# Kernel tuning notes

Hardware: AMD Instinct MI355X
Metric: run time of the kernel (lower is better)

## Reference

```python
import jax, jax.numpy as jnp
import numpy as np

N_NODES = 50000


def mean_aggregate(x, src, dst):
    # gather source features, scatter-sum to destinations, divide by in-degree
    msgs = x[src]                                             # [E, D]
    summed = jax.ops.segment_sum(msgs, dst, num_segments=N_NODES)  # [N, D]
    deg = jax.ops.segment_sum(jnp.ones_like(dst, dtype=x.dtype), dst,
                              num_segments=N_NODES)           # [N]
    return summed / jnp.clip(deg, 1.0)[:, None]


def sage_conv(x, src, dst, Wl, Wr, b):
    # PyG SAGEConv (aggr='mean'): lin_l(agg) + lin_r(x); bias only on lin_l
    agg = mean_aggregate(x, src, dst)
    return agg @ Wl + b + x @ Wr


def setup_inputs() -> dict:
    key = jax.random.key(0)
    ks = jax.random.split(key, 8)
    x = jax.random.normal(ks[0], (N_NODES, 64), dtype=jnp.float32)
    edge_index = jax.random.randint(ks[1], (2, 800000), 0, N_NODES, dtype=jnp.int32)
    W1l = jax.random.normal(ks[2], (64, 128), dtype=jnp.float32) * (1.0 / np.sqrt(64))
    W1r = jax.random.normal(ks[3], (64, 128), dtype=jnp.float32) * (1.0 / np.sqrt(64))
    b1 = jnp.zeros((128,), dtype=jnp.float32)
    W2l = jax.random.normal(ks[4], (128, 40), dtype=jnp.float32) * (1.0 / np.sqrt(128))
    W2r = jax.random.normal(ks[5], (128, 40), dtype=jnp.float32) * (1.0 / np.sqrt(128))
    b2 = jnp.zeros((40,), dtype=jnp.float32)
    return {"x": x, "edge_index": edge_index, "W1l": W1l, "W1r": W1r, "b1": b1,
            "W2l": W2l, "W2r": W2r, "b2": b2}


def reference(x, edge_index, W1l, W1r, b1, W2l, W2r, b2):
    src, dst = edge_index[0], edge_index[1]
    h = sage_conv(x, src, dst, W1l, W1r, b1)
    h = jax.nn.relu(h)
    # dropout p=0.5 is identity in eval mode (self.training=False)
    h = sage_conv(h, src, dst, W2l, W2r, b2)
    return h, jax.nn.log_softmax(h, axis=1)
```

## Files before the change

### kernel.cpp

```cpp
#include <hip/hip_runtime.h>
#include <hip/hip_bf16.h>
#include <math.h>

#define N_NODES 50000
#define N_EDGES 800000
#define D0 64
#define D1 128
#define D2 40

#define NB  256
#define NPB 196

typedef short s16x8 __attribute__((ext_vector_type(8)));
typedef float f32x4 __attribute__((ext_vector_type(4)));

static __device__ __forceinline__ unsigned short f2bf(float v) {
    __hip_bfloat16 hb = __float2bfloat16(v);
    return *(unsigned short*)&hb;
}

__global__ __launch_bounds__(256) void prep_kernel(
        const float* __restrict__ x, const int* __restrict__ dst,
        const float* __restrict__ W1l, const float* __restrict__ W1r,
        const float* __restrict__ W2l, const float* __restrict__ W2r,
        unsigned short* __restrict__ xh, int* __restrict__ hist,
        unsigned short* __restrict__ wpk1, unsigned short* __restrict__ wpk2,
        int E, int nCount, int nCast) {
    int b = blockIdx.x, t = threadIdx.x;
    if (b < nCount) {
        __shared__ int h[NB];
        h[t] = 0;
        __syncthreads();
        int e0 = b * 2048;
        for (int i = t; i < 2048; i += 256) {
            int e = e0 + i;
            if (e < E) atomicAdd(&h[(unsigned)dst[e] / NPB], 1);
        }
        __syncthreads();
        hist[b * NB + t] = h[t];
    } else if (b < nCount + nCast) {
        int i = ((b - nCount) * 256 + t) * 4;
        float4 v = *(const float4*)(x + i);
        unsigned o0 = (unsigned)f2bf(v.x) | ((unsigned)f2bf(v.y) << 16);
        unsigned o1 = (unsigned)f2bf(v.z) | ((unsigned)f2bf(v.w) << 16);
        uint2 pk; pk.x = o0; pk.y = o1;
        *(uint2*)(xh + i) = pk;
    } else if (b < nCount + nCast + 8) {
        int f = (b - nCount - nCast) * 4 + (t >> 6);
        int lane = t & 63;
        int nt = f & 7;
        int col = nt * 16 + (lane & 15);
        int kbase = (f >> 3) * 32 + (lane >> 4) * 8;
        unsigned short* o = wpk1 + ((size_t)f * 64 + lane) * 8;
#pragma unroll
        for (int j = 0; j < 8; ++j) {
            int k = kbase + j;
            float w = (k < 64) ? W1r[k * 128 + col] : W1l[(k - 64) * 128 + col];
            o[j] = f2bf(w);
        }
    } else {
        int f = (b - nCount - nCast - 8) * 4 + (t >> 6);
        if (f < 20) {
            int lane = t & 63;
            int nt = f % 5;
            int col = nt * 16 + (lane & 15);
            int kbase = (f / 5) * 32 + (lane >> 4) * 8;
            unsigned short* o = wpk2 + ((size_t)f * 64 + lane) * 8;
#pragma unroll
            for (int j = 0; j < 8; ++j) {
                int k = kbase + j;
                float w = (col < 40) ? W2l[k * 40 + col] : W2r[k * 40 + (col - 40)];
                o[j] = f2bf(w);
            }
        }
    }
}

__global__ void bucket_scan_kernel(const int* __restrict__ hist, int nCount,
                                   int* __restrict__ bbase, int* __restrict__ bcursor) {
    __shared__ int sd[NB];
    int t = threadIdx.x;
    int v = 0;
#pragma unroll 4
    for (int b = 0; b < nCount; ++b) v += hist[b * NB + t];
    sd[t] = v;
    __syncthreads();
    for (int off = 1; off < NB; off <<= 1) {
        int u = (t >= off) ? sd[t - off] : 0;
        __syncthreads();
        sd[t] += u;
        __syncthreads();
    }
    int ex = sd[t] - v;
    bbase[t] = ex;
    bcursor[t] = ex;
}

__global__ __launch_bounds__(256) void bucket_scatter_kernel(
        const int* __restrict__ src, const int* __restrict__ dst,
        int* __restrict__ bcursor, unsigned* __restrict__ ebuf, int E) {
    __shared__ int h[NB];
    __shared__ int base[NB];
    int t = threadIdx.x;
    int e0 = blockIdx.x * 4096;
    h[t] = 0;
    __syncthreads();
    for (int i = t; i < 4096; i += 256) {
        int e = e0 + i;
        if (e < E) atomicAdd(&h[(unsigned)dst[e] / NPB], 1);
    }
    __syncthreads();
    if (h[t] > 0) base[t] = atomicAdd(&bcursor[t], h[t]);
    h[t] = 0;
    __syncthreads();
    for (int i = t; i < 4096; i += 256) {
        int e = e0 + i;
        if (e < E) {
            unsigned d = (unsigned)dst[e];
            unsigned b = d / NPB;
            unsigned ld = d - b * NPB;
            int k = atomicAdd(&h[b], 1);
            ebuf[base[b] + k] = (ld << 17) | (unsigned)src[e];
        }
    }
}

__global__ __launch_bounds__(256) void bucket_fill_kernel(
        const unsigned* __restrict__ ebuf, const int* __restrict__ bbase,
        int* __restrict__ rowptr, int* __restrict__ csr, int E, int N) {
    __shared__ int cnt[256];
    __shared__ int sd[256];
    int b = blockIdx.x, t = threadIdx.x;
    int s0 = bbase[b];
    int s1 = (b < NB - 1) ? bbase[b + 1] : E;
    int lo = b * NPB;
    cnt[t] = 0;
    __syncthreads();
    for (int i = s0 + t; i < s1; i += 256)
        atomicAdd(&cnt[ebuf[i] >> 17], 1);
    __syncthreads();
    int v = cnt[t];
    sd[t] = v;
    __syncthreads();
    for (int off = 1; off < 256; off <<= 1) {
        int u = (t >= off) ? sd[t - off] : 0;
        __syncthreads();
        sd[t] += u;
        __syncthreads();
    }
    int ex = sd[t] - v;
    int node = lo + t;
    if (t < NPB && node < N) rowptr[node] = s0 + ex;
    cnt[t] = s0 + ex;
    __syncthreads();
    for (int i = s0 + t; i < s1; i += 256) {
        unsigned pk = ebuf[i];
        int p = atomicAdd(&cnt[pk >> 17], 1);
        csr[p] = (int)(pk & 0x1FFFFu);
    }
    if (b == NB - 1 && t == 0) rowptr[N] = E;
}


__global__ void agg1_kernel(const unsigned short* __restrict__ xh, const int* __restrict__ rowptr,
                            const int* __restrict__ csr, unsigned short* __restrict__ aggh, int N) {
    int wid = (blockIdx.x * blockDim.x + threadIdx.x) >> 6;
    int lane = threadIdx.x & 63;
    if (wid >= N) return;
    int beg = rowptr[wid], end = rowptr[wid + 1];
    int deg = end - beg;
    int l = lane & 7, g = lane >> 3;
    float acc[8];
#pragma unroll
    for (int k = 0; k < 8; ++k) acc[k] = 0.f;
    int jmax = (deg + 7) >> 3;
    for (int j = 0; j < jmax; j += 4) {
        int s[4]; float w[4];
#pragma unroll
        for (int u = 0; u < 4; ++u) {
            int slot = (j + u) * 8 + g;
            int e = beg + slot;
            e = (e < end) ? e : (end - 1);
            s[u] = csr[e];
            w[u] = (slot < deg) ? 1.f : 0.f;
        }
#pragma unroll
        for (int u = 0; u < 4; ++u) {
            uint4 v = *(const uint4*)(xh + (size_t)s[u] * D0 + l * 8);
            float f0 = __uint_as_float(v.x << 16), f1 = __uint_as_float(v.x & 0xffff0000u);
            float f2 = __uint_as_float(v.y << 16), f3 = __uint_as_float(v.y & 0xffff0000u);
            float f4 = __uint_as_float(v.z << 16), f5 = __uint_as_float(v.z & 0xffff0000u);
            float f6 = __uint_as_float(v.w << 16), f7 = __uint_as_float(v.w & 0xffff0000u);
            acc[0] = fmaf(w[u], f0, acc[0]); acc[1] = fmaf(w[u], f1, acc[1]);
            acc[2] = fmaf(w[u], f2, acc[2]); acc[3] = fmaf(w[u], f3, acc[3]);
            acc[4] = fmaf(w[u], f4, acc[4]); acc[5] = fmaf(w[u], f5, acc[5]);
            acc[6] = fmaf(w[u], f6, acc[6]); acc[7] = fmaf(w[u], f7, acc[7]);
        }
    }
#pragma unroll
    for (int off = 8; off <= 32; off <<= 1) {
#pragma unroll
        for (int k = 0; k < 8; ++k) acc[k] += __shfl_xor(acc[k], off);
    }
    float inv = 1.f / (float)max(deg, 1);
    if (g == 0) {
        unsigned o0 = (unsigned)f2bf(acc[0] * inv) | ((unsigned)f2bf(acc[1] * inv) << 16);
        unsigned o1 = (unsigned)f2bf(acc[2] * inv) | ((unsigned)f2bf(acc[3] * inv) << 16);
        unsigned o2 = (unsigned)f2bf(acc[4] * inv) | ((unsigned)f2bf(acc[5] * inv) << 16);
        unsigned o3 = (unsigned)f2bf(acc[6] * inv) | ((unsigned)f2bf(acc[7] * inv) << 16);
        uint4 pk; pk.x = o0; pk.y = o1; pk.z = o2; pk.w = o3;
        *(uint4*)(aggh + (size_t)wid * D0 + l * 8) = pk;
    }
}


__global__ void agg2_kernel(const unsigned short* __restrict__ p2h, const float* __restrict__ r2,
                            const int* __restrict__ rowptr, const int* __restrict__ csr,
                            float* __restrict__ out, float* __restrict__ out2, int N) {
    int wid = (blockIdx.x * blockDim.x + threadIdx.x) >> 6;
    int lane = threadIdx.x & 63;
    if (wid >= N) return;
    int beg = rowptr[wid], end = rowptr[wid + 1];
    int deg = end - beg;
    int g = lane / 10;
    int l = lane - g * 10;
    bool gv = g < 6;
    float ax = 0.f, ay = 0.f, az = 0.f, aw = 0.f;
    int jmax = (deg + 5) / 6;
    for (int j = 0; j < jmax; j += 4) {
        int s[4]; float w[4];
#pragma unroll
        for (int u = 0; u < 4; ++u) {
            int slot = (j + u) * 6 + g;
            int e = beg + slot;
            e = (e < end) ? e : (end - 1);
            s[u] = csr[e];
            w[u] = (gv && slot < deg) ? 1.f : 0.f;
        }
#pragma unroll
        for (int u = 0; u < 4; ++u) {
            uint2 v = *(const uint2*)(p2h + (size_t)s[u] * D2 + l * 4);
            float f0 = __uint_as_float(v.x << 16), f1 = __uint_as_float(v.x & 0xffff0000u);
            float f2 = __uint_as_float(v.y << 16), f3 = __uint_as_float(v.y & 0xffff0000u);
            ax = fmaf(w[u], f0, ax); ay = fmaf(w[u], f1, ay);
            az = fmaf(w[u], f2, az); aw = fmaf(w[u], f3, aw);
        }
    }
    {
        float bx = __shfl(ax, lane + 30), by = __shfl(ay, lane + 30),
              bz = __shfl(az, lane + 30), bw = __shfl(aw, lane + 30);
        if (g < 3) { ax += bx; ay += by; az += bz; aw += bw; }
        bx = __shfl(ax, lane + 20); by = __shfl(ay, lane + 20);
        bz = __shfl(az, lane + 20); bw = __shfl(aw, lane + 20);
        if (g == 0) { ax += bx; ay += by; az += bz; aw += bw; }
        bx = __shfl(ax, lane + 10); by = __shfl(ay, lane + 10);
        bz = __shfl(az, lane + 10); bw = __shfl(aw, lane + 10);
        if (g == 0) { ax += bx; ay += by; az += bz; aw += bw; }
    }
    float inv = 1.f / (float)max(deg, 1);
    bool wr = (lane < 10);
    float4 h2;
    if (wr) {
        float4 rr = *(const float4*)(r2 + (size_t)wid * D2 + lane * 4);
        h2.x = rr.x + ax * inv; h2.y = rr.y + ay * inv;
        h2.z = rr.z + az * inv; h2.w = rr.w + aw * inv;
        *(float4*)(out + (size_t)wid * D2 + lane * 4) = h2;
    }
    float m = wr ? fmaxf(fmaxf(h2.x, h2.y), fmaxf(h2.z, h2.w)) : -INFINITY;
#pragma unroll
    for (int off = 1; off < 64; off <<= 1) m = fmaxf(m, __shfl_xor(m, off));
    float s = 0.f;
    if (wr) s = expf(h2.x - m) + expf(h2.y - m) + expf(h2.z - m) + expf(h2.w - m);
#pragma unroll
    for (int off = 1; off < 64; off <<= 1) s += __shfl_xor(s, off);
    if (wr) {
        float lg = m + logf(s);
        float4 o; o.x = h2.x - lg; o.y = h2.y - lg; o.z = h2.z - lg; o.w = h2.w - lg;
        *(float4*)(out2 + (size_t)wid * D2 + lane * 4) = o;
    }
}

__global__ __launch_bounds__(256) void gemm1_mfma(
        const unsigned short* __restrict__ xh, const unsigned short* __restrict__ aggh,
        const unsigned short* __restrict__ Wpk, const float* __restrict__ b1,
        unsigned short* __restrict__ h, int N) {
    __shared__ __align__(16) unsigned short As[128 * 136];
    int t = threadIdx.x;
    int r0 = blockIdx.x * 128;
    for (int i = t; i < 2048; i += 256) {
        int r = i >> 4, c = i & 15;
        int gr = r0 + r; gr = (gr < N) ? gr : (N - 1);
        uint4 v = (c < 8) ? ((const uint4*)(xh + (size_t)gr * 64))[c]
                          : ((const uint4*)(aggh + (size_t)gr * 64))[c - 8];
        *(uint4*)(As + r * 136 + c * 8) = v;
    }
    __syncthreads();
    int w = t >> 6, lane = t & 63;
    int l15 = lane & 15, q = lane >> 4;
    f32x4 zero = {0.f, 0.f, 0.f, 0.f};
    f32x4 acc[2][8];
#pragma unroll
    for (int rt = 0; rt < 2; ++rt)
#pragma unroll
        for (int nt = 0; nt < 8; ++nt) acc[rt][nt] = zero;
    const unsigned short* abase = As + (w * 32 + l15) * 136 + q * 8;
#pragma unroll
    for (int ks = 0; ks < 4; ++ks) {
        s16x8 a0 = *(const s16x8*)(abase + ks * 32);
        s16x8 a1 = *(const s16x8*)(abase + 16 * 136 + ks * 32);
        s16x8 b[8];
#pragma unroll
        for (int nt = 0; nt < 8; ++nt)
            b[nt] = *(const s16x8*)(Wpk + ((size_t)(ks * 8 + nt) * 64 + lane) * 8);
#pragma unroll
        for (int nt = 0; nt < 8; ++nt) {
            acc[0][nt] = __builtin_amdgcn_mfma_f32_16x16x32_bf16(a0, b[nt], acc[0][nt], 0, 0, 0);
            acc[1][nt] = __builtin_amdgcn_mfma_f32_16x16x32_bf16(a1, b[nt], acc[1][nt], 0, 0, 0);
        }
    }
    int rbase = r0 + w * 32 + q * 4;
#pragma unroll
    for (int nt = 0; nt < 8; ++nt) {
        int col = nt * 16 + l15;
        float bias = b1[col];
#pragma unroll
        for (int rt = 0; rt < 2; ++rt) {
#pragma unroll
            for (int reg = 0; reg < 4; ++reg) {
                int row = rbase + rt * 16 + reg;
                if (row < N)
                    h[(size_t)row * 128 + col] = f2bf(fmaxf(acc[rt][nt][reg] + bias, 0.f));
            }
        }
    }
}

__global__ __launch_bounds__(256) void gemm2_mfma(
        const unsigned short* __restrict__ hq, const unsigned short* __restrict__ Wpk,
        const float* __restrict__ b2,
        unsigned short* __restrict__ p2h, float* __restrict__ r2, int N) {
    __shared__ __align__(16) unsigned short As[128 * 136];
    int t = threadIdx.x;
    int r0 = blockIdx.x * 128;
    for (int i = t; i < 2048; i += 256) {
        int r = i >> 4, c = i & 15;
        int gr = r0 + r; gr = (gr < N) ? gr : (N - 1);
        uint4 v = ((const uint4*)(hq + (size_t)gr * 128))[c];
        *(uint4*)(As + r * 136 + c * 8) = v;
    }
    __syncthreads();
    int w = t >> 6, lane = t & 63;
    int l15 = lane & 15, q = lane >> 4;
    f32x4 zero = {0.f, 0.f, 0.f, 0.f};
    f32x4 acc[2][5];
#pragma unroll
    for (int rt = 0; rt < 2; ++rt)
#pragma unroll
        for (int nt = 0; nt < 5; ++nt) acc[rt][nt] = zero;
    const unsigned short* abase = As + (w * 32 + l15) * 136 + q * 8;
#pragma unroll
    for (int ks = 0; ks < 4; ++ks) {
        s16x8 a0 = *(const s16x8*)(abase + ks * 32);
        s16x8 a1 = *(const s16x8*)(abase + 16 * 136 + ks * 32);
        s16x8 b[5];
#pragma unroll
        for (int nt = 0; nt < 5; ++nt)
            b[nt] = *(const s16x8*)(Wpk + ((size_t)(ks * 5 + nt) * 64 + lane) * 8);
#pragma unroll
        for (int nt = 0; nt < 5; ++nt) {
            acc[0][nt] = __builtin_amdgcn_mfma_f32_16x16x32_bf16(a0, b[nt], acc[0][nt], 0, 0, 0);
            acc[1][nt] = __builtin_amdgcn_mfma_f32_16x16x32_bf16(a1, b[nt], acc[1][nt], 0, 0, 0);
        }
    }
    int rbase = r0 + w * 32 + q * 4;
#pragma unroll
    for (int nt = 0; nt < 5; ++nt) {
        int col = nt * 16 + l15;
        bool isp = col < 40;
        int oc = isp ? col : (col - 40);
        float bias = isp ? 0.f : b2[oc];
#pragma unroll
        for (int rt = 0; rt < 2; ++rt) {
#pragma unroll
            for (int reg = 0; reg < 4; ++reg) {
                int row = rbase + rt * 16 + reg;
                if (row < N) {
                    float v = acc[rt][nt][reg] + bias;
                    if (isp) p2h[(size_t)row * 40 + oc] = f2bf(v);
                    else     r2[(size_t)row * 40 + oc] = v;
                }
            }
        }
    }
}


extern "C" void kernel_launch(void* const* d_in, const int* in_sizes, int n_in,
                              void* d_out, int out_size, void* d_ws, size_t ws_size,
                              hipStream_t stream) {
    const float* x   = (const float*)d_in[0];
    const int*   ei  = (const int*)d_in[1];
    const float* W1l = (const float*)d_in[2];
    const float* W1r = (const float*)d_in[3];
    const float* b1  = (const float*)d_in[4];
    const float* W2l = (const float*)d_in[5];
    const float* W2r = (const float*)d_in[6];
    const float* b2  = (const float*)d_in[7];
    float* out = (float*)d_out;

    const int N = N_NODES;
    const int E = in_sizes[1] / 2;
    const int* src = ei;
    const int* dst = ei + E;

    char* p = (char*)d_ws;
    auto alloc = [&](size_t bytes) -> void* {
        void* r = (void*)p;
        p += (bytes + 255) & ~(size_t)255;
        return r;
    };
    const int nCount = (E + 2047) / 2048;
    const int nCast  = (N * D0) / 1024;

    int*      rowptr  = (int*)alloc((size_t)(N + 1) * 4);
    int*      csr     = (int*)alloc((size_t)E * 4);
    unsigned* ebuf    = (unsigned*)alloc((size_t)E * 4);
    int*      hist    = (int*)alloc((size_t)nCount * NB * 4);
    int*      bbase   = (int*)alloc(NB * 4);
    int*      bcursor = (int*)alloc(NB * 4);
    unsigned short* xh    = (unsigned short*)alloc((size_t)N * D0 * 2);
    unsigned short* aggh  = (unsigned short*)alloc((size_t)N * D0 * 2);
    unsigned short* hbuf  = (unsigned short*)alloc((size_t)N * D1 * 2);
    unsigned short* wpk1  = (unsigned short*)alloc((size_t)32 * 64 * 8 * 2);
    unsigned short* wpk2  = (unsigned short*)alloc((size_t)20 * 64 * 8 * 2);
    unsigned short* p2h   = (unsigned short*)alloc((size_t)N * D2 * 2);
    float* r2buf = (float*)alloc((size_t)N * D2 * 4);

    prep_kernel<<<nCount + nCast + 8 + 5, 256, 0, stream>>>(
        x, dst, W1l, W1r, W2l, W2r, xh, hist, wpk1, wpk2, E, nCount, nCast);
    bucket_scan_kernel<<<1, NB, 0, stream>>>(hist, nCount, bbase, bcursor);
    bucket_scatter_kernel<<<(E + 4095) / 4096, 256, 0, stream>>>(src, dst, bcursor, ebuf, E);
    bucket_fill_kernel<<<NB, 256, 0, stream>>>(ebuf, bbase, rowptr, csr, E, N);

    agg1_kernel<<<(N * 64 + 255) / 256, 256, 0, stream>>>(xh, rowptr, csr, aggh, N);
    gemm1_mfma<<<(N + 127) / 128, 256, 0, stream>>>(xh, aggh, wpk1, b1, hbuf, N);

    gemm2_mfma<<<(N + 127) / 128, 256, 0, stream>>>(hbuf, wpk2, b2, p2h, r2buf, N);
    agg2_kernel<<<(N * 64 + 255) / 256, 256, 0, stream>>>(p2h, r2buf, rowptr, csr,
                                                          out, out + (size_t)N * D2, N);
}
```

Before: 201.1 us.

## Fuse both GEMMs via LDS, widen agg2 rows, and peel masked tail in aggregations

Merges gemm1 and gemm2 into one kernel that keeps the ReLU'd hidden tile in shared memory, so the N×128 bf16 hidden buffer never goes through global memory and one launch is saved. The layer-2 projected features are stored padded to 64 bf16 per row, so agg2 can use 16-byte loads with 5 lanes per row and 12 edges per wave step. Both aggregation loops now handle full chunks without masking or clamping and keep the masked path only for the last chunk. The padded layout adds unused bytes per row, and agg2 gets a longer shuffle reduction over 8 accumulators.

```diff
diff --git a/kernel.cpp b/kernel.cpp
--- a/kernel.cpp
+++ b/kernel.cpp
@@ -174,28 +174,45 @@
 #pragma unroll
     for (int k = 0; k < 8; ++k) acc[k] = 0.f;
     int jmax = (deg + 7) >> 3;
-    for (int j = 0; j < jmax; j += 4) {
-        int s[4]; float w[4];
-#pragma unroll
-        for (int u = 0; u < 4; ++u) {
-            int slot = (j + u) * 8 + g;
-            int e = beg + slot;
-            e = (e < end) ? e : (end - 1);
-            s[u] = csr[e];
-            w[u] = (slot < deg) ? 1.f : 0.f;
-        }
-#pragma unroll
-        for (int u = 0; u < 4; ++u) {
-            uint4 v = *(const uint4*)(xh + (size_t)s[u] * D0 + l * 8);
-            float f0 = __uint_as_float(v.x << 16), f1 = __uint_as_float(v.x & 0xffff0000u);
-            float f2 = __uint_as_float(v.y << 16), f3 = __uint_as_float(v.y & 0xffff0000u);
-            float f4 = __uint_as_float(v.z << 16), f5 = __uint_as_float(v.z & 0xffff0000u);
-            float f6 = __uint_as_float(v.w << 16), f7 = __uint_as_float(v.w & 0xffff0000u);
-            acc[0] = fmaf(w[u], f0, acc[0]); acc[1] = fmaf(w[u], f1, acc[1]);
-            acc[2] = fmaf(w[u], f2, acc[2]); acc[3] = fmaf(w[u], f3, acc[3]);
-            acc[4] = fmaf(w[u], f4, acc[4]); acc[5] = fmaf(w[u], f5, acc[5]);
-            acc[6] = fmaf(w[u], f6, acc[6]); acc[7] = fmaf(w[u], f7, acc[7]);
-        }
+    int full = jmax - 1;
+    int j = 0;
+    for (; j + 2 <= full; j += 2) {
+        int s0 = csr[beg + j * 8 + g];
+        int s1 = csr[beg + (j + 1) * 8 + g];
+        uint4 v0 = *(const uint4*)(xh + (size_t)s0 * D0 + l * 8);
+        uint4 v1 = *(const uint4*)(xh + (size_t)s1 * D0 + l * 8);
+        acc[0] += __uint_as_float(v0.x << 16);          acc[1] += __uint_as_float(v0.x & 0xffff0000u);
+        acc[2] += __uint_as_float(v0.y << 16);          acc[3] += __uint_as_float(v0.y & 0xffff0000u);
+        acc[4] += __uint_as_float(v0.z << 16);          acc[5] += __uint_as_float(v0.z & 0xffff0000u);
+        acc[6] += __uint_as_float(v0.w << 16);          acc[7] += __uint_as_float(v0.w & 0xffff0000u);
+        acc[0] += __uint_as_float(v1.x << 16);          acc[1] += __uint_as_float(v1.x & 0xffff0000u);
+        acc[2] += __uint_as_float(v1.y << 16);          acc[3] += __uint_as_float(v1.y & 0xffff0000u);
+        acc[4] += __uint_as_float(v1.z << 16);          acc[5] += __uint_as_float(v1.z & 0xffff0000u);
+        acc[6] += __uint_as_float(v1.w << 16);          acc[7] += __uint_as_float(v1.w & 0xffff0000u);
+    }
+    if (j < full) {
+        int s0 = csr[beg + j * 8 + g];
+        uint4 v0 = *(const uint4*)(xh + (size_t)s0 * D0 + l * 8);
+        acc[0] += __uint_as_float(v0.x << 16);          acc[1] += __uint_as_float(v0.x & 0xffff0000u);
+        acc[2] += __uint_as_float(v0.y << 16);          acc[3] += __uint_as_float(v0.y & 0xffff0000u);
+        acc[4] += __uint_as_float(v0.z << 16);          acc[5] += __uint_as_float(v0.z & 0xffff0000u);
+        acc[6] += __uint_as_float(v0.w << 16);          acc[7] += __uint_as_float(v0.w & 0xffff0000u);
+    }
+    if (jmax > 0) {
+        int slot = full * 8 + g;
+        int e = beg + slot;
+        e = (e < end) ? e : (end - 1);
+        int s0 = csr[e];
+        float w = (slot < deg) ? 1.f : 0.f;
+        uint4 v0 = *(const uint4*)(xh + (size_t)s0 * D0 + l * 8);
+        acc[0] = fmaf(w, __uint_as_float(v0.x << 16), acc[0]);
+        acc[1] = fmaf(w, __uint_as_float(v0.x & 0xffff0000u), acc[1]);
+        acc[2] = fmaf(w, __uint_as_float(v0.y << 16), acc[2]);
+        acc[3] = fmaf(w, __uint_as_float(v0.y & 0xffff0000u), acc[3]);
+        acc[4] = fmaf(w, __uint_as_float(v0.z << 16), acc[4]);
+        acc[5] = fmaf(w, __uint_as_float(v0.z & 0xffff0000u), acc[5]);
+        acc[6] = fmaf(w, __uint_as_float(v0.w << 16), acc[6]);
+        acc[7] = fmaf(w, __uint_as_float(v0.w & 0xffff0000u), acc[7]);
     }
 #pragma unroll
     for (int off = 8; off <= 32; off <<= 1) {
@@ -222,68 +239,113 @@
     if (wid >= N) return;
     int beg = rowptr[wid], end = rowptr[wid + 1];
     int deg = end - beg;
-    int g = lane / 10;
-    int l = lane - g * 10;
-    bool gv = g < 6;
-    float ax = 0.f, ay = 0.f, az = 0.f, aw = 0.f;
-    int jmax = (deg + 5) / 6;
-    for (int j = 0; j < jmax; j += 4) {
-        int s[4]; float w[4];
-#pragma unroll
-        for (int u = 0; u < 4; ++u) {
-            int slot = (j + u) * 6 + g;
-            int e = beg + slot;
-            e = (e < end) ? e : (end - 1);
-            s[u] = csr[e];
-            w[u] = (gv && slot < deg) ? 1.f : 0.f;
-        }
-#pragma unroll
-        for (int u = 0; u < 4; ++u) {
-            uint2 v = *(const uint2*)(p2h + (size_t)s[u] * D2 + l * 4);
-            float f0 = __uint_as_float(v.x << 16), f1 = __uint_as_float(v.x & 0xffff0000u);
-            float f2 = __uint_as_float(v.y << 16), f3 = __uint_as_float(v.y & 0xffff0000u);
-            ax = fmaf(w[u], f0, ax); ay = fmaf(w[u], f1, ay);
-            az = fmaf(w[u], f2, az); aw = fmaf(w[u], f3, aw);
-        }
+    int g = lane / 5;
+    int l = lane - g * 5;
+    bool gv = g < 12;
+    float a[8];
+#pragma unroll
+    for (int k = 0; k < 8; ++k) a[k] = 0.f;
+    int jmax = (deg + 11) / 12;
+    int full = jmax - 1;
+    int j = 0;
+    for (; j + 2 <= full; j += 2) {
+        int s0 = csr[beg + j * 12 + g];
+        int s1 = csr[beg + (j + 1) * 12 + g];
+        uint4 v0 = *(const uint4*)(p2h + (size_t)s0 * 64 + l * 8);
+        uint4 v1 = *(const uint4*)(p2h + (size_t)s1 * 64 + l * 8);
+        if (gv) {
+            a[0] += __uint_as_float(v0.x << 16);  a[1] += __uint_as_float(v0.x & 0xffff0000u);
+            a[2] += __uint_as_float(v0.y << 16);  a[3] += __uint_as_float(v0.y & 0xffff0000u);
+            a[4] += __uint_as_float(v0.z << 16);  a[5] += __uint_as_float(v0.z & 0xffff0000u);
+            a[6] += __uint_as_float(v0.w << 16);  a[7] += __uint_as_float(v0.w & 0xffff0000u);
+            a[0] += __uint_as_float(v1.x << 16);  a[1] += __uint_as_float(v1.x & 0xffff0000u);
+            a[2] += __uint_as_float(v1.y << 16);  a[3] += __uint_as_float(v1.y & 0xffff0000u);
+            a[4] += __uint_as_float(v1.z << 16);  a[5] += __uint_as_float(v1.z & 0xffff0000u);
+            a[6] += __uint_as_float(v1.w << 16);  a[7] += __uint_as_float(v1.w & 0xffff0000u);
+        }
+    }
+    if (j < full) {
+        int s0 = csr[beg + j * 12 + g];
+        uint4 v0 = *(const uint4*)(p2h + (size_t)s0 * 64 + l * 8);
+        if (gv) {
+            a[0] += __uint_as_float(v0.x << 16);  a[1] += __uint_as_float(v0.x & 0xffff0000u);
+            a[2] += __uint_as_float(v0.y << 16);  a[3] += __uint_as_float(v0.y & 0xffff0000u);
+            a[4] += __uint_as_float(v0.z << 16);  a[5] += __uint_as_float(v0.z & 0xffff0000u);
+            a[6] += __uint_as_float(v0.w << 16);  a[7] += __uint_as_float(v0.w & 0xffff0000u);
+        }
+    }
+    if (jmax > 0) {
+        int slot = full * 12 + g;
+        int e = beg + slot;
+        e = (e < end) ? e : (end - 1);
+        int s0 = csr[e];
+        float w = (gv && slot < deg) ? 1.f : 0.f;
+        uint4 v0 = *(const uint4*)(p2h + (size_t)s0 * 64 + l * 8);
+        a[0] = fmaf(w, __uint_as_float(v0.x << 16), a[0]);
+        a[1] = fmaf(w, __uint_as_float(v0.x & 0xffff0000u), a[1]);
+        a[2] = fmaf(w, __uint_as_float(v0.y << 16), a[2]);
+        a[3] = fmaf(w, __uint_as_float(v0.y & 0xffff0000u), a[3]);
+        a[4] = fmaf(w, __uint_as_float(v0.z << 16), a[4]);
+        a[5] = fmaf(w, __uint_as_float(v0.z & 0xffff0000u), a[5]);
+        a[6] = fmaf(w, __uint_as_float(v0.w << 16), a[6]);
+        a[7] = fmaf(w, __uint_as_float(v0.w & 0xffff0000u), a[7]);
     }
     {
-        float bx = __shfl(ax, lane + 30), by = __shfl(ay, lane + 30),
-              bz = __shfl(az, lane + 30), bw = __shfl(aw, lane + 30);
-        if (g < 3) { ax += bx; ay += by; az += bz; aw += bw; }
-        bx = __shfl(ax, lane + 20); by = __shfl(ay, lane + 20);
-        bz = __shfl(az, lane + 20); bw = __shfl(aw, lane + 20);
-        if (g == 0) { ax += bx; ay += by; az += bz; aw += bw; }
-        bx = __shfl(ax, lane + 10); by = __shfl(ay, lane + 10);
-        bz = __shfl(az, lane + 10); bw = __shfl(aw, lane + 10);
-        if (g == 0) { ax += bx; ay += by; az += bz; aw += bw; }
+        float b0;
+#pragma unroll
+        for (int k = 0; k < 8; ++k) { b0 = __shfl(a[k], lane + 30); if (g < 6) a[k] += b0; }
+#pragma unroll
+        for (int k = 0; k < 8; ++k) { b0 = __shfl(a[k], lane + 15); if (g < 3) a[k] += b0; }
+#pragma unroll
+        for (int k = 0; k < 8; ++k) {
+            float b1 = __shfl(a[k], lane + 5);
+            float b2 = __shfl(a[k], lane + 10);
+            if (g == 0) a[k] += b1 + b2;
+        }
     }
     float inv = 1.f / (float)max(deg, 1);
-    bool wr = (lane < 10);
-    float4 h2;
+    bool wr = (lane < 5);
+    float h2[8];
     if (wr) {
-        float4 rr = *(const float4*)(r2 + (size_t)wid * D2 + lane * 4);
-        h2.x = rr.x + ax * inv; h2.y = rr.y + ay * inv;
-        h2.z = rr.z + az * inv; h2.w = rr.w + aw * inv;
-        *(float4*)(out + (size_t)wid * D2 + lane * 4) = h2;
-    }
-    float m = wr ? fmaxf(fmaxf(h2.x, h2.y), fmaxf(h2.z, h2.w)) : -INFINITY;
+        float4 ra = *(const float4*)(r2 + (size_t)wid * D2 + lane * 8);
+        float4 rb = *(const float4*)(r2 + (size_t)wid * D2 + lane * 8 + 4);
+        h2[0] = ra.x + a[0] * inv; h2[1] = ra.y + a[1] * inv;
+        h2[2] = ra.z + a[2] * inv; h2[3] = ra.w + a[3] * inv;
+        h2[4] = rb.x + a[4] * inv; h2[5] = rb.y + a[5] * inv;
+        h2[6] = rb.z + a[6] * inv; h2[7] = rb.w + a[7] * inv;
+        float4 oa; oa.x = h2[0]; oa.y = h2[1]; oa.z = h2[2]; oa.w = h2[3];
+        float4 ob; ob.x = h2[4]; ob.y = h2[5]; ob.z = h2[6]; ob.w = h2[7];
+        *(float4*)(out + (size_t)wid * D2 + lane * 8) = oa;
+        *(float4*)(out + (size_t)wid * D2 + lane * 8 + 4) = ob;
+    }
+    float m = -INFINITY;
+    if (wr) {
+#pragma unroll
+        for (int k = 0; k < 8; ++k) m = fmaxf(m, h2[k]);
+    }
 #pragma unroll
     for (int off = 1; off < 64; off <<= 1) m = fmaxf(m, __shfl_xor(m, off));
     float s = 0.f;
-    if (wr) s = expf(h2.x - m) + expf(h2.y - m) + expf(h2.z - m) + expf(h2.w - m);
+    if (wr) {
+#pragma unroll
+        for (int k = 0; k < 8; ++k) s += expf(h2[k] - m);
+    }
 #pragma unroll
     for (int off = 1; off < 64; off <<= 1) s += __shfl_xor(s, off);
     if (wr) {
         float lg = m + logf(s);
-        float4 o; o.x = h2.x - lg; o.y = h2.y - lg; o.z = h2.z - lg; o.w = h2.w - lg;
-        *(float4*)(out2 + (size_t)wid * D2 + lane * 4) = o;
-    }
-}
-
-__global__ __launch_bounds__(256) void gemm1_mfma(
+        float4 oa; oa.x = h2[0] - lg; oa.y = h2[1] - lg; oa.z = h2[2] - lg; oa.w = h2[3] - lg;
+        float4 ob; ob.x = h2[4] - lg; ob.y = h2[5] - lg; ob.z = h2[6] - lg; ob.w = h2[7] - lg;
+        *(float4*)(out2 + (size_t)wid * D2 + lane * 8) = oa;
+        *(float4*)(out2 + (size_t)wid * D2 + lane * 8 + 4) = ob;
+    }
+}
+
+__global__ __launch_bounds__(256) void gemm_fused(
         const unsigned short* __restrict__ xh, const unsigned short* __restrict__ aggh,
-        const unsigned short* __restrict__ Wpk, const float* __restrict__ b1,
-        unsigned short* __restrict__ h, int N) {
+        const unsigned short* __restrict__ Wpk1, const unsigned short* __restrict__ Wpk2,
+        const float* __restrict__ b1, const float* __restrict__ b2,
+        unsigned short* __restrict__ p2h, float* __restrict__ r2, int N) {
     __shared__ __align__(16) unsigned short As[128 * 136];
     int t = threadIdx.x;
     int r0 = blockIdx.x * 128;
@@ -298,12 +360,13 @@
     int w = t >> 6, lane = t & 63;
     int l15 = lane & 15, q = lane >> 4;
     f32x4 zero = {0.f, 0.f, 0.f, 0.f};
+    const unsigned short* abase = As + (w * 32 + l15) * 136 + q * 8;
+
     f32x4 acc[2][8];
 #pragma unroll
     for (int rt = 0; rt < 2; ++rt)
 #pragma unroll
         for (int nt = 0; nt < 8; ++nt) acc[rt][nt] = zero;
-    const unsigned short* abase = As + (w * 32 + l15) * 136 + q * 8;
 #pragma unroll
     for (int ks = 0; ks < 4; ++ks) {
         s16x8 a0 = *(const s16x8*)(abase + ks * 32);
@@ -311,14 +374,15 @@
         s16x8 b[8];
 #pragma unroll
         for (int nt = 0; nt < 8; ++nt)
-            b[nt] = *(const s16x8*)(Wpk + ((size_t)(ks * 8 + nt) * 64 + lane) * 8);
+            b[nt] = *(const s16x8*)(Wpk1 + ((size_t)(ks * 8 + nt) * 64 + lane) * 8);
 #pragma unroll
         for (int nt = 0; nt < 8; ++nt) {
             acc[0][nt] = __builtin_amdgcn_mfma_f32_16x16x32_bf16(a0, b[nt], acc[0][nt], 0, 0, 0);
             acc[1][nt] = __builtin_amdgcn_mfma_f32_16x16x32_bf16(a1, b[nt], acc[1][nt], 0, 0, 0);
         }
     }
-    int rbase = r0 + w * 32 + q * 4;
+    __syncthreads();
+    int rloc = w * 32 + q * 4;
 #pragma unroll
     for (int nt = 0; nt < 8; ++nt) {
         int col = nt * 16 + l15;
@@ -327,37 +391,17 @@
         for (int rt = 0; rt < 2; ++rt) {
 #pragma unroll
             for (int reg = 0; reg < 4; ++reg) {
-                int row = rbase + rt * 16 + reg;
-                if (row < N)
-                    h[(size_t)row * 128 + col] = f2bf(fmaxf(acc[rt][nt][reg] + bias, 0.f));
+                int row = rloc + rt * 16 + reg;
+                As[row * 136 + col] = f2bf(fmaxf(acc[rt][nt][reg] + bias, 0.f));
             }
         }
     }
-}
-
-__global__ __launch_bounds__(256) void gemm2_mfma(
-        const unsigned short* __restrict__ hq, const unsigned short* __restrict__ Wpk,
-        const float* __restrict__ b2,
-        unsigned short* __restrict__ p2h, float* __restrict__ r2, int N) {
-    __shared__ __align__(16) unsigned short As[128 * 136];
-    int t = threadIdx.x;
-    int r0 = blockIdx.x * 128;
-    for (int i = t; i < 2048; i += 256) {
-        int r = i >> 4, c = i & 15;
-        int gr = r0 + r; gr = (gr < N) ? gr : (N - 1);
-        uint4 v = ((const uint4*)(hq + (size_t)gr * 128))[c];
-        *(uint4*)(As + r * 136 + c * 8) = v;
-    }
-    __syncthreads();
-    int w = t >> 6, lane = t & 63;
-    int l15 = lane & 15, q = lane >> 4;
-    f32x4 zero = {0.f, 0.f, 0.f, 0.f};
-    f32x4 acc[2][5];
+    __syncthreads();
+    f32x4 acc2[2][5];
 #pragma unroll
     for (int rt = 0; rt < 2; ++rt)
 #pragma unroll
-        for (int nt = 0; nt < 5; ++nt) acc[rt][nt] = zero;
-    const unsigned short* abase = As + (w * 32 + l15) * 136 + q * 8;
+        for (int nt = 0; nt < 5; ++nt) acc2[rt][nt] = zero;
 #pragma unroll
     for (int ks = 0; ks < 4; ++ks) {
         s16x8 a0 = *(const s16x8*)(abase + ks * 32);
@@ -365,11 +409,11 @@
         s16x8 b[5];
 #pragma unroll
         for (int nt = 0; nt < 5; ++nt)
-            b[nt] = *(const s16x8*)(Wpk + ((size_t)(ks * 5 + nt) * 64 + lane) * 8);
+            b[nt] = *(const s16x8*)(Wpk2 + ((size_t)(ks * 5 + nt) * 64 + lane) * 8);
 #pragma unroll
         for (int nt = 0; nt < 5; ++nt) {
-            acc[0][nt] = __builtin_amdgcn_mfma_f32_16x16x32_bf16(a0, b[nt], acc[0][nt], 0, 0, 0);
-            acc[1][nt] = __builtin_amdgcn_mfma_f32_16x16x32_bf16(a1, b[nt], acc[1][nt], 0, 0, 0);
+            acc2[0][nt] = __builtin_amdgcn_mfma_f32_16x16x32_bf16(a0, b[nt], acc2[0][nt], 0, 0, 0);
+            acc2[1][nt] = __builtin_amdgcn_mfma_f32_16x16x32_bf16(a1, b[nt], acc2[1][nt], 0, 0, 0);
         }
     }
     int rbase = r0 + w * 32 + q * 4;
@@ -385,9 +429,9 @@
             for (int reg = 0; reg < 4; ++reg) {
                 int row = rbase + rt * 16 + reg;
                 if (row < N) {
-                    float v = acc[rt][nt][reg] + bias;
-                    if (isp) p2h[(size_t)row * 40 + oc] = f2bf(v);
-                    else     r2[(size_t)row * 40 + oc] = v;
+                    float v = acc2[rt][nt][reg] + bias;
+                    if (isp) p2h[(size_t)row * 64 + oc] = f2bf(v);
+                    else     r2[(size_t)row * D2 + oc] = v;
                 }
             }
         }
@@ -430,10 +474,9 @@
     int*      bcursor = (int*)alloc(NB * 4);
     unsigned short* xh    = (unsigned short*)alloc((size_t)N * D0 * 2);
     unsigned short* aggh  = (unsigned short*)alloc((size_t)N * D0 * 2);
-    unsigned short* hbuf  = (unsigned short*)alloc((size_t)N * D1 * 2);
     unsigned short* wpk1  = (unsigned short*)alloc((size_t)32 * 64 * 8 * 2);
     unsigned short* wpk2  = (unsigned short*)alloc((size_t)20 * 64 * 8 * 2);
-    unsigned short* p2h   = (unsigned short*)alloc((size_t)N * D2 * 2);
+    unsigned short* p2h   = (unsigned short*)alloc((size_t)N * 64 * 2);
     float* r2buf = (float*)alloc((size_t)N * D2 * 4);
 
     prep_kernel<<<nCount + nCast + 8 + 5, 256, 0, stream>>>(
@@ -443,9 +486,9 @@
     bucket_fill_kernel<<<NB, 256, 0, stream>>>(ebuf, bbase, rowptr, csr, E, N);
 
     agg1_kernel<<<(N * 64 + 255) / 256, 256, 0, stream>>>(xh, rowptr, csr, aggh, N);
-    gemm1_mfma<<<(N + 127) / 128, 256, 0, stream>>>(xh, aggh, wpk1, b1, hbuf, N);
-
-    gemm2_mfma<<<(N + 127) / 128, 256, 0, stream>>>(hbuf, wpk2, b2, p2h, r2buf, N);
+    gemm_fused<<<(N + 127) / 128, 256, 0, stream>>>(xh, aggh, wpk1, wpk2, b1, b2,
+                                                    p2h, r2buf, N);
+
     agg2_kernel<<<(N * 64 + 255) / 256, 256, 0, stream>>>(p2h, r2buf, rowptr, csr,
                                                           out, out + (size_t)N * D2, N);
 }
```

Result: no change. 199.2 us (-1.0%).
